# Kernel optimization log

Measured on AMD Instinct MI355X. Metric: run time of the kernel, lower is better.

Reference implementation:

```python
import jax, jax.numpy as jnp
import numpy as np

EPS = 1e-8
LN_EPS = 1e-5
DIM, NHEADS = 512, 8
HEAD_DIM = DIM // NHEADS
SCALE = HEAD_DIM ** -0.5
ROLE_VOCAB = 8


def _layernorm(x, g, b):
    mu = x.mean(-1, keepdims=True)
    var = ((x - mu) ** 2).mean(-1, keepdims=True)
    return (x - mu) * jax.lax.rsqrt(var + LN_EPS) * g + b


def setup_inputs() -> dict:
    key = jax.random.key(0)
    ks = jax.random.split(key, 16)
    B, K, L, D = 8, 4, 1024, DIM
    s = 1.0 / np.sqrt(D)
    return {
        "state_repr": jax.random.normal(ks[0], (B, K, L, D), jnp.float32),
        "residue_mask": jax.random.randint(ks[1], (B, K, L), 0, 2) > 0,
        "state_weights": jax.random.uniform(ks[2], (B, K), jnp.float32),
        "state_roles": jax.random.randint(ks[3], (B, K), 0, ROLE_VOCAB),
        "state_present_mask": jnp.ones((B, K), dtype=bool),
        "role_emb": jax.random.normal(ks[4], (ROLE_VOCAB, D), jnp.float32),
        "Wq": jax.random.normal(ks[5], (D, D), jnp.float32) * s,
        "Wk": jax.random.normal(ks[6], (D, D), jnp.float32) * s,
        "Wv": jax.random.normal(ks[7], (D, D), jnp.float32) * s,
        "Wo": jax.random.normal(ks[8], (D, D), jnp.float32) * s,
        "ln1_g": jnp.ones((3 * D,), jnp.float32),
        "ln1_b": jnp.zeros((3 * D,), jnp.float32),
        "Wg1": jax.random.normal(ks[9], (D, 3 * D), jnp.float32) / np.sqrt(3 * D),
        "bg1": jnp.zeros((D,), jnp.float32),
        "Wg2": jax.random.normal(ks[10], (D, D), jnp.float32) * s,
        "bg2": jnp.zeros((D,), jnp.float32),
        "norm_g": jnp.ones((D,), jnp.float32),
        "norm_b": jnp.zeros((D,), jnp.float32),
    }


def _forward(state_repr, residue_mask, state_weights, state_roles, state_present_mask,
             role_emb, Wq, Wk, Wv, Wo, ln1_g, ln1_b, Wg1, bg1, Wg2, bg2, norm_g, norm_b):
    B, K, L, D = state_repr.shape
    H, hd = NHEADS, HEAD_DIM
    roles = jnp.maximum(state_roles, 0)
    role_e = role_emb[roles][:, :, None, :]                       # [B,K,1,D]
    valid = residue_mask & state_present_mask[:, :, None]          # [B,K,L]

    # normalized state weights
    pres = state_present_mask.astype(jnp.float32)
    w = state_weights.astype(jnp.float32) * pres
    denom = w.sum(1, keepdims=True)
    fallback = pres / jnp.maximum(pres.sum(1, keepdims=True), 1.0)
    nsw = jnp.where(denom > EPS, w / jnp.maximum(denom, EPS), fallback)  # [B,K]

    x = (state_repr + role_e) * valid[..., None]
    x = x.transpose(0, 2, 1, 3)                                    # [B,L,K,D]
    valid_rlk = valid.transpose(0, 2, 1)                           # [B,L,K]

    def proj(W):  # torch Linear: y = x @ W.T
        return (x @ W.T).reshape(B, L, K, H, hd).transpose(0, 1, 3, 2, 4)  # [B,L,H,K,hd]

    q, k, v = proj(Wq), proj(Wk), proj(Wv)
    logits = jnp.einsum('blhqd,blhkd->blhqk', q, k) * SCALE
    logits = logits + jnp.log(jnp.maximum(nsw, EPS))[:, None, None, None, :]
    key_mask = valid_rlk[:, :, None, None, :]                      # [B,L,1,1,K]
    logits = jnp.where(key_mask, logits, -jnp.inf)
    attn = jax.nn.softmax(logits, axis=-1)
    attn = jnp.nan_to_num(attn, nan=0.0, posinf=0.0, neginf=0.0)
    attn_out = jnp.einsum('blhqk,blhkd->blhqd', attn, v)
    attn_out = attn_out.transpose(0, 1, 3, 2, 4).reshape(B, L, K, D)
    attn_out = (attn_out @ Wo.T) * valid_rlk[..., None]

    swr = nsw[:, None, :] * valid_rlk.astype(jnp.float32)          # [B,L,K]
    swr = swr / jnp.maximum(swr.sum(-1, keepdims=True), EPS)
    weighted_mean = jnp.sum(x * swr[..., None], axis=2)            # [B,L,D]
    attn_pooled = jnp.sum(attn_out * swr[..., None], axis=2)

    max_in = jnp.where(valid_rlk[..., None], x, -1e9)
    max_feat = max_in.max(axis=2)
    has_any = valid_rlk.any(axis=2, keepdims=True)
    max_feat = jnp.where(has_any, max_feat, 0.0)

    fusion_base = 0.5 * (attn_pooled + weighted_mean)
    gate_in = jnp.concatenate([attn_pooled, weighted_mean, max_feat], axis=-1)
    h = _layernorm(gate_in, ln1_g, ln1_b)
    h = jax.nn.gelu(h @ Wg1.T + bg1, approximate=False)
    gate = jax.nn.sigmoid(h @ Wg2.T + bg2)
    fused = gate * fusion_base + (1.0 - gate) * max_feat
    fused = _layernorm(fused + weighted_mean, norm_g, norm_b)

    attn_mean = attn.mean(axis=(2, 3))                             # [B,L,K]
    return fused, attn_pooled, weighted_mean, max_feat, attn_mean, nsw


def reference(state_repr, residue_mask, state_weights, state_roles, state_present_mask,
              role_emb, Wq, Wk, Wv, Wo, ln1_g, ln1_b, Wg1, bg1, Wg2, bg2, norm_g, norm_b):
    return _forward(state_repr, residue_mask, state_weights, state_roles, state_present_mask,
                    role_emb, Wq, Wk, Wv, Wo, ln1_g, ln1_b, Wg1, bg1, Wg2, bg2, norm_g, norm_b)
```

## Files before the change

### kernel.cpp

```cpp
#include <hip/hip_runtime.h>
#include <math.h>

#define BB 8
#define KK 4
#define LL 1024
#define DD 512
#define HD 64
#define D3 1536
#define MM (BB*LL*KK)
#define BL (BB*LL)
#define SCALE 0.125f
#define EPSF 1e-8f
#define LN_EPSF 1e-5f

typedef _Float16 hfrag __attribute__((ext_vector_type(8)));
typedef float f32x4 __attribute__((ext_vector_type(4)));

__device__ __forceinline__ unsigned short f2h(float f) {
    _Float16 h = (_Float16)f;
    unsigned short u; __builtin_memcpy(&u, &h, 2); return u;
}
__device__ __forceinline__ float h2f(unsigned short u) {
    _Float16 h; __builtin_memcpy(&h, &u, 2); return (float)h;
}

__device__ __forceinline__ void glds16(const unsigned short* g, unsigned short* l) {
    __builtin_amdgcn_global_load_lds(
        (const __attribute__((address_space(1))) void*)g,
        (__attribute__((address_space(3))) void*)l, 16, 0, 0);
}

__device__ __forceinline__ void nsw_compute(const float* sw, const int* pres,
                                            int b, float* nswv) {
    float w[KK], pr[KK]; float denom = 0.f, ps = 0.f;
    #pragma unroll
    for (int k = 0; k < KK; ++k) {
        pr[k] = pres[b*KK + k] ? 1.f : 0.f;
        w[k]  = sw[b*KK + k] * pr[k];
        denom += w[k]; ps += pr[k];
    }
    #pragma unroll
    for (int k = 0; k < KK; ++k)
        nswv[k] = (denom > EPSF) ? w[k] / fmaxf(denom, EPSF)
                                 : pr[k] / fmaxf(ps, 1.f);
}

#define WSZ 262144
#define OG1 1048576
#define OG2 1835008
#define WTOT 2097152
__global__ __launch_bounds__(256) void cvt_weights(
        const float* __restrict__ Wq, const float* __restrict__ Wk,
        const float* __restrict__ Wv, const float* __restrict__ Wo,
        const float* __restrict__ Wg1, const float* __restrict__ Wg2,
        unsigned short* __restrict__ dst) {
    int t = blockIdx.x * 256 + threadIdx.x;
    int e = t * 4;
    const float* src; int off;
    if      (e < WSZ)    { src = Wq;  off = e; }
    else if (e < 2*WSZ)  { src = Wk;  off = e - WSZ; }
    else if (e < 3*WSZ)  { src = Wv;  off = e - 2*WSZ; }
    else if (e < OG1)    { src = Wo;  off = e - 3*WSZ; }
    else if (e < OG2)    { src = Wg1; off = e - OG1; }
    else                 { src = Wg2; off = e - OG2; }
    float4 v = *(const float4*)(src + off);
    ushort4 o;
    o.x = f2h(v.x); o.y = f2h(v.y); o.z = f2h(v.z); o.w = f2h(v.w);
    *(ushort4*)(dst + e) = o;
}

__global__ __launch_bounds__(256) void buildx_kernel(
        const float* __restrict__ SR, const int* __restrict__ residue,
        const int* __restrict__ pres, const int* __restrict__ roles,
        const float* __restrict__ role_emb, const float* __restrict__ sw,
        unsigned short* __restrict__ Xh, float* __restrict__ rowmask,
        float* __restrict__ out_wm, float* __restrict__ out_mx,
        float* __restrict__ f_nsw) {
    int t  = blockIdx.x * 256 + threadIdx.x;
    int bl = t >> 7;
    int d4 = (t & 127) << 2;
    int b  = bl >> 10, l = bl & 1023;
    float nswv[KK];
    nsw_compute(sw, pres, b, nswv);
    float mk[KK], swr[KK];
    float ssum = 0.f, many = 0.f;
    #pragma unroll
    for (int k = 0; k < KK; ++k) {
        int bk = b*KK + k;
        bool valid = (residue[(size_t)bk*LL + l] != 0) && (pres[bk] != 0);
        mk[k]  = valid ? 1.f : 0.f;
        swr[k] = nswv[k] * mk[k];
        ssum += swr[k]; many += mk[k];
    }
    float inv = 1.f / fmaxf(ssum, EPSF);
    bool hasany = many > 0.5f;
    float wmx = 0.f, wmy = 0.f, wmz = 0.f, wmw = 0.f;
    float mxx = -1e9f, mxy = -1e9f, mxz = -1e9f, mxw = -1e9f;
    #pragma unroll
    for (int k = 0; k < KK; ++k) {
        int bk = b*KK + k;
        int role = roles[bk]; if (role < 0) role = 0;
        float4 sr = *(const float4*)(SR + ((size_t)bk*LL + l)*DD + d4);
        float4 re = *(const float4*)(role_emb + (size_t)role*DD + d4);
        float xx = (sr.x + re.x)*mk[k], xy = (sr.y + re.y)*mk[k];
        float xz = (sr.z + re.z)*mk[k], xw = (sr.w + re.w)*mk[k];
        ushort4 xs; xs.x = f2h(xx); xs.y = f2h(xy); xs.z = f2h(xz); xs.w = f2h(xw);
        *(ushort4*)(Xh + (size_t)(bl*KK + k)*DD + d4) = xs;
        float s = swr[k]*inv;
        wmx = fmaf(xx, s, wmx); wmy = fmaf(xy, s, wmy);
        wmz = fmaf(xz, s, wmz); wmw = fmaf(xw, s, wmw);
        if (mk[k] > 0.5f) {
            mxx = fmaxf(mxx, xx); mxy = fmaxf(mxy, xy);
            mxz = fmaxf(mxz, xz); mxw = fmaxf(mxw, xw);
        }
    }
    if (!hasany) { mxx = mxy = mxz = mxw = 0.f; }
    float4 wmv; wmv.x = wmx; wmv.y = wmy; wmv.z = wmz; wmv.w = wmw;
    float4 mxv; mxv.x = mxx; mxv.y = mxy; mxv.z = mxz; mxv.w = mxw;
    *(float4*)(out_wm + (size_t)bl*DD + d4) = wmv;
    *(float4*)(out_mx + (size_t)bl*DD + d4) = mxv;
    if (d4 == 0) {
        #pragma unroll
        for (int k = 0; k < KK; ++k) rowmask[bl*KK + k] = mk[k];
    }
    if (blockIdx.x == 0 && threadIdx.x < BB*KK) {
        int bb = threadIdx.x >> 2, kk2 = threadIdx.x & 3;
        float nv[KK];
        nsw_compute(sw, pres, bb, nv);
        f_nsw[threadIdx.x] = nv[kk2];
    }
}

__global__ __launch_bounds__(512, 4) void gemm_qkv_8p(
        const unsigned short* __restrict__ A, const unsigned short* __restrict__ W,
        unsigned short* __restrict__ Cbase) {
    __shared__ __align__(16) unsigned short smem[36864];
    const int tid  = threadIdx.x;
    const int wave = tid >> 6, lane = tid & 63;
    const int id = blockIdx.x;
    const int wg = (id & 7) * 192 + (id >> 3);
    const int m0 = (wg / 12) * 256;
    const int n0 = (wg % 12) * 128;
    const int wm = wave >> 1, wn = wave & 1;
    const int fr = lane & 15, q = lane >> 4;
    const int srow = tid >> 2, scc = tid & 3;
    const int sswz = (scc ^ ((srow >> 1) & 3)) << 3;
    const unsigned short* Ag0 = A + (size_t)(m0 + srow)*512 + sswz;
    const unsigned short* Ag1 = Ag0 + (size_t)128*512;
    const unsigned short* Wg0 = W + (size_t)(n0 + srow)*512 + sswz;
    const int lA0 = tid << 3;
    const int lA1 = (tid + 512) << 3;
    int aoff[4], boff[4];
    #pragma unroll
    for (int mf = 0; mf < 4; ++mf) {
        int row = (wm << 6) + (mf << 4) + fr;
        aoff[mf] = (row << 5) + ((q ^ ((row >> 1) & 3)) << 3);
    }
    #pragma unroll
    for (int nf = 0; nf < 4; ++nf) {
        int row = (wn << 6) + (nf << 4) + fr;
        boff[nf] = (row << 5) + ((q ^ ((row >> 1) & 3)) << 3);
    }
    f32x4 acc[4][4] = {};

#define VMWAIT(N) asm volatile("s_waitcnt vmcnt(" #N ")" ::: "memory")
#define STAGE(tt) do { unsigned short* _d = smem + ((tt) % 3) * 12288; \
        const int _ko = (tt) << 5; \
        glds16(Ag0 + _ko, _d + lA0); glds16(Ag1 + _ko, _d + lA1); \
        glds16(Wg0 + _ko, _d + 8192 + lA0); } while (0)
#define MFROW(ai, areg) \
        acc[ai][0] = __builtin_amdgcn_mfma_f32_16x16x32_f16(areg, b0, acc[ai][0], 0, 0, 0); \
        acc[ai][1] = __builtin_amdgcn_mfma_f32_16x16x32_f16(areg, b1, acc[ai][1], 0, 0, 0); \
        acc[ai][2] = __builtin_amdgcn_mfma_f32_16x16x32_f16(areg, b2, acc[ai][2], 0, 0, 0); \
        acc[ai][3] = __builtin_amdgcn_mfma_f32_16x16x32_f16(areg, b3, acc[ai][3], 0, 0, 0);
#define TILE(t, STG, VM) do { \
        const unsigned short* _Ab = smem + ((t) % 3) * 12288; \
        const unsigned short* _Bb = _Ab + 8192; \
        VMWAIT(VM); \
        __builtin_amdgcn_s_barrier(); \
        __builtin_amdgcn_sched_barrier(0); \
        hfrag b0 = *(const hfrag*)(_Bb + boff[0]); \
        hfrag b1 = *(const hfrag*)(_Bb + boff[1]); \
        hfrag b2 = *(const hfrag*)(_Bb + boff[2]); \
        hfrag b3 = *(const hfrag*)(_Bb + boff[3]); \
        hfrag a0_ = *(const hfrag*)(_Ab + aoff[0]); \
        hfrag a1_ = *(const hfrag*)(_Ab + aoff[1]); \
        hfrag a2_ = *(const hfrag*)(_Ab + aoff[2]); \
        hfrag a3_ = *(const hfrag*)(_Ab + aoff[3]); \
        if (STG) STAGE((t) + 2); \
        __builtin_amdgcn_s_setprio(1); \
        MFROW(0, a0_) MFROW(1, a1_) MFROW(2, a2_) MFROW(3, a3_) \
        __builtin_amdgcn_s_setprio(0); \
    } while (0)

    STAGE(0); STAGE(1);
    #pragma unroll
    for (int t = 0; t < 14; ++t) TILE(t, 1, 3);
    TILE(14, 0, 3);
    TILE(15, 0, 0);
#undef TILE
#undef MFROW
#undef STAGE
#undef VMWAIT

    const int gc0 = n0 + (wn << 6);
    const int seg = gc0 >> 9;
    unsigned short* Cs = Cbase + (size_t)seg * ((size_t)MM * 512);
    const int cb = gc0 & 511;
    #pragma unroll
    for (int mf = 0; mf < 4; ++mf) {
        const int grow = m0 + (wm << 6) + (mf << 4) + (q << 2);
        #pragma unroll
        for (int nf = 0; nf < 4; ++nf) {
            const int col = cb + (nf << 4) + fr;
            #pragma unroll
            for (int r = 0; r < 4; ++r)
                Cs[(size_t)(grow + r) * 512 + col] = f2h(acc[mf][nf][r]);
        }
    }
}

__global__ __launch_bounds__(512, 4) void wo_gemm(
        const unsigned short* __restrict__ A,
        const unsigned short* __restrict__ W,
        const float* __restrict__ sw, const int* __restrict__ pres,
        const float* __restrict__ rmask, float* __restrict__ out_ap) {
    __shared__ __align__(16) unsigned short smem[36864];
    const int tid  = threadIdx.x;
    const int wave = tid >> 6, lane = tid & 63;
    const int id = blockIdx.x;
    const int wg = (id & 7) * 64 + (id >> 3);
    const int m0 = (wg >> 2) * 256;
    const int n0 = (wg & 3) * 128;
    const int wm = wave >> 1, wn = wave & 1;
    const int fr = lane & 15, q = lane >> 4;
    const int srow = tid >> 2, scc = tid & 3;
    const int sswz = (scc ^ ((srow >> 1) & 3)) << 3;
    const unsigned short* Ag0 = A + (size_t)(m0 + srow)*512 + sswz;
    const unsigned short* Ag1 = Ag0 + (size_t)128*512;
    const unsigned short* Wg0 = W + (size_t)(n0 + srow)*512 + sswz;
    const int lA0 = tid << 3;
    const int lA1 = (tid + 512) << 3;
    int aoff[4], boff[4];
    #pragma unroll
    for (int mf = 0; mf < 4; ++mf) {
        int row = (wm << 6) + (mf << 4) + fr;
        aoff[mf] = (row << 5) + ((q ^ ((row >> 1) & 3)) << 3);
    }
    #pragma unroll
    for (int nf = 0; nf < 4; ++nf) {
        int row = (wn << 6) + (nf << 4) + fr;
        boff[nf] = (row << 5) + ((q ^ ((row >> 1) & 3)) << 3);
    }
    f32x4 acc[4][4] = {};

#define VMWAIT(N) asm volatile("s_waitcnt vmcnt(" #N ")" ::: "memory")
#define STAGE(tt) do { unsigned short* _d = smem + ((tt) % 3) * 12288; \
        const int _ko = (tt) << 5; \
        glds16(Ag0 + _ko, _d + lA0); glds16(Ag1 + _ko, _d + lA1); \
        glds16(Wg0 + _ko, _d + 8192 + lA0); } while (0)
#define MFROW(ai, areg) \
        acc[ai][0] = __builtin_amdgcn_mfma_f32_16x16x32_f16(areg, b0, acc[ai][0], 0, 0, 0); \
        acc[ai][1] = __builtin_amdgcn_mfma_f32_16x16x32_f16(areg, b1, acc[ai][1], 0, 0, 0); \
        acc[ai][2] = __builtin_amdgcn_mfma_f32_16x16x32_f16(areg, b2, acc[ai][2], 0, 0, 0); \
        acc[ai][3] = __builtin_amdgcn_mfma_f32_16x16x32_f16(areg, b3, acc[ai][3], 0, 0, 0);
#define TILE(t, STG, VM) do { \
        const unsigned short* _Ab = smem + ((t) % 3) * 12288; \
        const unsigned short* _Bb = _Ab + 8192; \
        VMWAIT(VM); \
        __builtin_amdgcn_s_barrier(); \
        __builtin_amdgcn_sched_barrier(0); \
        hfrag b0 = *(const hfrag*)(_Bb + boff[0]); \
        hfrag b1 = *(const hfrag*)(_Bb + boff[1]); \
        hfrag b2 = *(const hfrag*)(_Bb + boff[2]); \
        hfrag b3 = *(const hfrag*)(_Bb + boff[3]); \
        hfrag a0_ = *(const hfrag*)(_Ab + aoff[0]); \
        hfrag a1_ = *(const hfrag*)(_Ab + aoff[1]); \
        hfrag a2_ = *(const hfrag*)(_Ab + aoff[2]); \
        hfrag a3_ = *(const hfrag*)(_Ab + aoff[3]); \
        if (STG) STAGE((t) + 2); \
        __builtin_amdgcn_s_setprio(1); \
        MFROW(0, a0_) MFROW(1, a1_) MFROW(2, a2_) MFROW(3, a3_) \
        __builtin_amdgcn_s_setprio(0); \
    } while (0)

    STAGE(0); STAGE(1);
    #pragma unroll
    for (int t = 0; t < 14; ++t) TILE(t, 1, 3);
    TILE(14, 0, 3);
    TILE(15, 0, 0);
#undef TILE
#undef MFROW
#undef STAGE
#undef VMWAIT

    const int b = (m0 >> 2) >> 10;
    float nv[KK];
    nsw_compute(sw, pres, b, nv);
    #pragma unroll
    for (int mf = 0; mf < 4; ++mf) {
        const int grow = m0 + (wm << 6) + (mf << 4) + (q << 2);
        const int bl = grow >> 2;
        float s4[KK]; float ssum = 0.f;
        #pragma unroll
        for (int k = 0; k < KK; ++k) { s4[k] = nv[k] * rmask[bl*4 + k]; ssum += s4[k]; }
        const float inv = 1.f / fmaxf(ssum, EPSF);
        #pragma unroll
        for (int nf = 0; nf < 4; ++nf) {
            const int col = n0 + (wn << 6) + (nf << 4) + fr;
            float ap = 0.f;
            #pragma unroll
            for (int r = 0; r < KK; ++r) ap = fmaf(s4[r]*inv, acc[mf][nf][r], ap);
            out_ap[(size_t)bl*512 + col] = ap;
        }
    }
}

__global__ __launch_bounds__(256) void ln1_kernel(
        const float* __restrict__ ap, const float* __restrict__ wm,
        const float* __restrict__ mx, const float* __restrict__ g,
        const float* __restrict__ bvec, unsigned short* __restrict__ hin) {
    const int bl = blockIdx.x * 4 + (threadIdx.x >> 6);
    const int lane = threadIdx.x & 63;
    const int c0 = lane * 8;
    float4 v[3][2];
    const float* srcs[3] = { ap + (size_t)bl*512 + c0,
                             wm + (size_t)bl*512 + c0,
                             mx + (size_t)bl*512 + c0 };
    float s = 0.f, s2 = 0.f;
    #pragma unroll
    for (int sg = 0; sg < 3; ++sg) {
        v[sg][0] = *(const float4*)(srcs[sg]);
        v[sg][1] = *(const float4*)(srcs[sg] + 4);
        #pragma unroll
        for (int e = 0; e < 8; ++e) {
            float x = ((const float*)v[sg])[e];
            s += x; s2 += x*x;
        }
    }
    #pragma unroll
    for (int o = 1; o < 64; o <<= 1) {
        s  += __shfl_xor(s,  o, 64);
        s2 += __shfl_xor(s2, o, 64);
    }
    const float mu = s * (1.f/(float)D3);
    const float var = s2 * (1.f/(float)D3) - mu*mu;
    const float rstd = rsqrtf(var + LN_EPSF);
    #pragma unroll
    for (int sg = 0; sg < 3; ++sg) {
        const int gofs = sg*512 + c0;
        #pragma unroll
        for (int h = 0; h < 2; ++h) {
            float4 g4 = *(const float4*)(g + gofs + h*4);
            float4 b4 = *(const float4*)(bvec + gofs + h*4);
            const float* sv = (const float*)&v[sg][h];
            ushort4 o4;
            o4.x = f2h((sv[0]-mu)*rstd*g4.x + b4.x);
            o4.y = f2h((sv[1]-mu)*rstd*g4.y + b4.y);
            o4.z = f2h((sv[2]-mu)*rstd*g4.z + b4.z);
            o4.w = f2h((sv[3]-mu)*rstd*g4.w + b4.w);
            *(ushort4*)(hin + (size_t)bl*D3 + gofs + h*4) = o4;
        }
    }
}

__global__ __launch_bounds__(256, 3) void gemm_g1(
        const unsigned short* __restrict__ A, const unsigned short* __restrict__ W,
        unsigned short* __restrict__ C, const float* __restrict__ bias) {
    __shared__ __align__(16) unsigned short smem[24576];
    const int tid  = threadIdx.x;
    const int wave = tid >> 6, lane = tid & 63;
    const int id = blockIdx.x;
    const int wg = (id & 7) * 32 + (id >> 3);
    const int m0 = (wg >> 2) * 128;
    const int n0 = (wg & 3) * 128;
    const int wm = wave >> 1, wn = wave & 1;
    const int fr = lane & 15, q = lane >> 4;
    const int srow = tid >> 2, scc = tid & 3;
    const int sswz = (scc ^ ((srow >> 1) & 3)) << 3;
    const unsigned short* Ag0 = A + (size_t)(m0 + srow)*D3 + sswz;
    const unsigned short* Ag1 = Ag0 + (size_t)64*D3;
    const unsigned short* Wg0 = W + (size_t)(n0 + srow)*D3 + sswz;
    const unsigned short* Wg1p = Wg0 + (size_t)64*D3;
    const int lA0 = tid << 3;
    const int lA1 = (tid + 256) << 3;
    int aoff[4], boff[4];
    #pragma unroll
    for (int mf = 0; mf < 4; ++mf) {
        int row = (wm << 6) + (mf << 4) + fr;
        aoff[mf] = (row << 5) + ((q ^ ((row >> 1) & 3)) << 3);
    }
    #pragma unroll
    for (int nf = 0; nf < 4; ++nf) {
        int row = (wn << 6) + (nf << 4) + fr;
        boff[nf] = (row << 5) + ((q ^ ((row >> 1) & 3)) << 3);
    }
    f32x4 acc[4][4] = {};

#define VMWAIT(N) asm volatile("s_waitcnt vmcnt(" #N ")" ::: "memory")
#define STAGE(tt) do { unsigned short* _d = smem + ((tt) % 3) * 8192; \
        const int _ko = (tt) << 5; \
        glds16(Ag0 + _ko, _d + lA0); glds16(Ag1 + _ko, _d + lA1); \
        glds16(Wg0 + _ko, _d + 4096 + lA0); glds16(Wg1p + _ko, _d + 4096 + lA1); } while (0)
#define MFROW(ai, areg) \
        acc[ai][0] = __builtin_amdgcn_mfma_f32_16x16x32_f16(areg, b0, acc[ai][0], 0, 0, 0); \
        acc[ai][1] = __builtin_amdgcn_mfma_f32_16x16x32_f16(areg, b1, acc[ai][1], 0, 0, 0); \
        acc[ai][2] = __builtin_amdgcn_mfma_f32_16x16x32_f16(areg, b2, acc[ai][2], 0, 0, 0); \
        acc[ai][3] = __builtin_amdgcn_mfma_f32_16x16x32_f16(areg, b3, acc[ai][3], 0, 0, 0);
#define TILE(t, STG, VM) do { \
        const unsigned short* _Ab = smem + ((t) % 3) * 8192; \
        const unsigned short* _Bb = _Ab + 4096; \
        VMWAIT(VM); \
        __builtin_amdgcn_s_barrier(); \
        __builtin_amdgcn_sched_barrier(0); \
        hfrag b0 = *(const hfrag*)(_Bb + boff[0]); \
        hfrag b1 = *(const hfrag*)(_Bb + boff[1]); \
        hfrag b2 = *(const hfrag*)(_Bb + boff[2]); \
        hfrag b3 = *(const hfrag*)(_Bb + boff[3]); \
        hfrag a0_ = *(const hfrag*)(_Ab + aoff[0]); \
        hfrag a1_ = *(const hfrag*)(_Ab + aoff[1]); \
        hfrag a2_ = *(const hfrag*)(_Ab + aoff[2]); \
        hfrag a3_ = *(const hfrag*)(_Ab + aoff[3]); \
        if (STG) STAGE((t) + 2); \
        __builtin_amdgcn_s_setprio(1); \
        MFROW(0, a0_) MFROW(1, a1_) MFROW(2, a2_) MFROW(3, a3_) \
        __builtin_amdgcn_s_setprio(0); \
    } while (0)

    STAGE(0); STAGE(1);
    #pragma unroll 3
    for (int t = 0; t < 46; ++t) TILE(t, 1, 4);
    TILE(46, 0, 4);
    TILE(47, 0, 0);
#undef TILE
#undef MFROW
#undef STAGE
#undef VMWAIT

    #pragma unroll
    for (int mf = 0; mf < 4; ++mf) {
        const int grow = m0 + (wm << 6) + (mf << 4) + (q << 2);
        #pragma unroll
        for (int nf = 0; nf < 4; ++nf) {
            const int col = n0 + (wn << 6) + (nf << 4) + fr;
            const float bv = bias[col];
            #pragma unroll
            for (int r = 0; r < 4; ++r) {
                float v = acc[mf][nf][r] + bv;
                v = 0.5f * v * (1.f + erff(v * 0.70710678118654752f));
                C[(size_t)(grow + r) * 512 + col] = f2h(v);
            }
        }
    }
}

__global__ __launch_bounds__(256, 3) void wg2_gemm(
        const unsigned short* __restrict__ A,
        const unsigned short* __restrict__ W,
        const float* __restrict__ bg2,
        const float* __restrict__ in_ap, const float* __restrict__ in_wm,
        const float* __restrict__ in_mx, float* __restrict__ pre) {
    __shared__ __align__(16) unsigned short smem[24576];
    const int tid  = threadIdx.x;
    const int wave = tid >> 6, lane = tid & 63;
    const int id = blockIdx.x;
    const int wg = (id & 7) * 32 + (id >> 3);
    const int m0 = (wg >> 2) * 128;
    const int n0 = (wg & 3) * 128;
    const int wm = wave >> 1, wn = wave & 1;
    const int fr = lane & 15, q = lane >> 4;
    const int srow = tid >> 2, scc = tid & 3;
    const int sswz = (scc ^ ((srow >> 1) & 3)) << 3;
    const unsigned short* Ag0 = A + (size_t)(m0 + srow)*512 + sswz;
    const unsigned short* Ag1 = Ag0 + (size_t)64*512;
    const unsigned short* Wg0 = W + (size_t)(n0 + srow)*512 + sswz;
    const unsigned short* Wg1p = Wg0 + (size_t)64*512;
    const int lA0 = tid << 3;
    const int lA1 = (tid + 256) << 3;
    int aoff[4], boff[4];
    #pragma unroll
    for (int mf = 0; mf < 4; ++mf) {
        int row = (wm << 6) + (mf << 4) + fr;
        aoff[mf] = (row << 5) + ((q ^ ((row >> 1) & 3)) << 3);
    }
    #pragma unroll
    for (int nf = 0; nf < 4; ++nf) {
        int row = (wn << 6) + (nf << 4) + fr;
        boff[nf] = (row << 5) + ((q ^ ((row >> 1) & 3)) << 3);
    }
    f32x4 acc[4][4] = {};

#define VMWAIT(N) asm volatile("s_waitcnt vmcnt(" #N ")" ::: "memory")
#define STAGE(tt) do { unsigned short* _d = smem + ((tt) % 3) * 8192; \
        const int _ko = (tt) << 5; \
        glds16(Ag0 + _ko, _d + lA0); glds16(Ag1 + _ko, _d + lA1); \
        glds16(Wg0 + _ko, _d + 4096 + lA0); glds16(Wg1p + _ko, _d + 4096 + lA1); } while (0)
#define MFROW(ai, areg) \
        acc[ai][0] = __builtin_amdgcn_mfma_f32_16x16x32_f16(areg, b0, acc[ai][0], 0, 0, 0); \
        acc[ai][1] = __builtin_amdgcn_mfma_f32_16x16x32_f16(areg, b1, acc[ai][1], 0, 0, 0); \
        acc[ai][2] = __builtin_amdgcn_mfma_f32_16x16x32_f16(areg, b2, acc[ai][2], 0, 0, 0); \
        acc[ai][3] = __builtin_amdgcn_mfma_f32_16x16x32_f16(areg, b3, acc[ai][3], 0, 0, 0);
#define TILE(t, STG, VM) do { \
        const unsigned short* _Ab = smem + ((t) % 3) * 8192; \
        const unsigned short* _Bb = _Ab + 4096; \
        VMWAIT(VM); \
        __builtin_amdgcn_s_barrier(); \
        __builtin_amdgcn_sched_barrier(0); \
        hfrag b0 = *(const hfrag*)(_Bb + boff[0]); \
        hfrag b1 = *(const hfrag*)(_Bb + boff[1]); \
        hfrag b2 = *(const hfrag*)(_Bb + boff[2]); \
        hfrag b3 = *(const hfrag*)(_Bb + boff[3]); \
        hfrag a0_ = *(const hfrag*)(_Ab + aoff[0]); \
        hfrag a1_ = *(const hfrag*)(_Ab + aoff[1]); \
        hfrag a2_ = *(const hfrag*)(_Ab + aoff[2]); \
        hfrag a3_ = *(const hfrag*)(_Ab + aoff[3]); \
        if (STG) STAGE((t) + 2); \
        __builtin_amdgcn_s_setprio(1); \
        MFROW(0, a0_) MFROW(1, a1_) MFROW(2, a2_) MFROW(3, a3_) \
        __builtin_amdgcn_s_setprio(0); \
    } while (0)

    STAGE(0); STAGE(1);
    #pragma unroll
    for (int t = 0; t < 14; ++t) TILE(t, 1, 4);
    TILE(14, 0, 4);
    TILE(15, 0, 0);
#undef TILE
#undef MFROW
#undef STAGE
#undef VMWAIT

    #pragma unroll
    for (int mf = 0; mf < 4; ++mf) {
        const int grow = m0 + (wm << 6) + (mf << 4) + (q << 2);
        #pragma unroll
        for (int nf = 0; nf < 4; ++nf) {
            const int col = n0 + (wn << 6) + (nf << 4) + fr;
            const float bv = bg2[col];
            #pragma unroll
            for (int r = 0; r < 4; ++r) {
                const int row = grow + r;
                float g = 1.f / (1.f + expf(-(acc[mf][nf][r] + bv)));
                float ap = in_ap[(size_t)row*512 + col];
                float wmv = in_wm[(size_t)row*512 + col];
                float mxv = in_mx[(size_t)row*512 + col];
                pre[(size_t)row*512 + col] = g*0.5f*(ap + wmv) + (1.f - g)*mxv + wmv;
            }
        }
    }
}

__global__ __launch_bounds__(256) void final_ln_kernel(
        const float* __restrict__ pre, const float* __restrict__ ng,
        const float* __restrict__ nb, float* __restrict__ fused) {
    const int row = blockIdx.x * 4 + (threadIdx.x >> 6);
    const int lane = threadIdx.x & 63;
    const int c0 = lane * 8;
    float4 p0 = *(const float4*)(pre + (size_t)row*512 + c0);
    float4 p1 = *(const float4*)(pre + (size_t)row*512 + c0 + 4);
    float s = 0.f, s2 = 0.f;
    const float* pv = (const float*)&p0;
    #pragma unroll
    for (int e = 0; e < 4; ++e) { s += pv[e]; s2 += pv[e]*pv[e]; }
    pv = (const float*)&p1;
    #pragma unroll
    for (int e = 0; e < 4; ++e) { s += pv[e]; s2 += pv[e]*pv[e]; }
    #pragma unroll
    for (int o = 1; o < 64; o <<= 1) {
        s  += __shfl_xor(s,  o, 64);
        s2 += __shfl_xor(s2, o, 64);
    }
    const float mu = s * (1.f/(float)DD);
    const float var = s2 * (1.f/(float)DD) - mu*mu;
    const float rstd = rsqrtf(var + LN_EPSF);
    float4 g0 = *(const float4*)(ng + c0), g1 = *(const float4*)(ng + c0 + 4);
    float4 b0 = *(const float4*)(nb + c0), b1 = *(const float4*)(nb + c0 + 4);
    float4 o0, o1;
    o0.x = (p0.x-mu)*rstd*g0.x + b0.x; o0.y = (p0.y-mu)*rstd*g0.y + b0.y;
    o0.z = (p0.z-mu)*rstd*g0.z + b0.z; o0.w = (p0.w-mu)*rstd*g0.w + b0.w;
    o1.x = (p1.x-mu)*rstd*g1.x + b1.x; o1.y = (p1.y-mu)*rstd*g1.y + b1.y;
    o1.z = (p1.z-mu)*rstd*g1.z + b1.z; o1.w = (p1.w-mu)*rstd*g1.w + b1.w;
    *(float4*)(fused + (size_t)row*512 + c0) = o0;
    *(float4*)(fused + (size_t)row*512 + c0 + 4) = o1;
}

__global__ __launch_bounds__(256) void attn_kernel(
        unsigned short* Qb ,
        const unsigned short* __restrict__ Kb, const unsigned short* __restrict__ Vb,
        const float* __restrict__ sw, const int* __restrict__ pres,
        const float* __restrict__ rowmask,
        float* __restrict__ attn_mean_out) {
    __shared__ float att[128];
    __shared__ float lw[KK], mk[KK];
    int bl = blockIdx.x, b = bl >> 10, mb = bl * KK;
    int tid = threadIdx.x;
    if (tid < KK) {
        float nv[KK];
        nsw_compute(sw, pres, b, nv);
        lw[tid] = logf(fmaxf(nv[tid], EPSF));
        mk[tid] = rowmask[mb + tid];
    }
    __syncthreads();
    if (tid < 128) {
        int h = tid >> 4, i = (tid >> 2) & 3, j = tid & 3;
        const unsigned short* qp = Qb + (size_t)(mb + i)*DD + h*HD;
        const unsigned short* kp = Kb + (size_t)(mb + j)*DD + h*HD;
        float s = 0.f;
        #pragma unroll
        for (int c = 0; c < 8; ++c) {
            hfrag qv = *(const hfrag*)(qp + c*8);
            hfrag kv = *(const hfrag*)(kp + c*8);
            #pragma unroll
            for (int e = 0; e < 8; ++e)
                s = fmaf((float)qv[e], (float)kv[e], s);
        }
        float lg = s * SCALE + lw[j];
        att[tid] = (mk[j] > 0.5f) ? lg : -INFINITY;
    }
    __syncthreads();
    if (tid < 32) {
        int base = tid * 4;
        float l0 = att[base], l1 = att[base+1], l2 = att[base+2], l3 = att[base+3];
        float m = fmaxf(fmaxf(l0, l1), fmaxf(l2, l3));
        if (m == -INFINITY) {
            att[base] = att[base+1] = att[base+2] = att[base+3] = 0.f;
        } else {
            float e0 = expf(l0 - m), e1 = expf(l1 - m), e2 = expf(l2 - m), e3 = expf(l3 - m);
            float inv = 1.f / (e0 + e1 + e2 + e3);
            att[base] = e0*inv; att[base+1] = e1*inv; att[base+2] = e2*inv; att[base+3] = e3*inv;
        }
    }
    __syncthreads();
    if (tid < KK) {
        float s = 0.f;
        for (int hi = 0; hi < 32; ++hi) s += att[hi*4 + tid];
        attn_mean_out[(size_t)bl*KK + tid] = s * (1.f/32.f);
    }
    #pragma unroll
    for (int p = 0; p < 4; ++p) {
        int idx = p*256 + tid;
        int i = idx >> 8, d2 = (idx & 255) << 1, h = d2 >> 6;
        float s0 = 0.f, s1 = 0.f;
        #pragma unroll
        for (int j = 0; j < KK; ++j) {
            float aj = att[h*16 + i*4 + j];
            ushort2 vv = *(const ushort2*)(Vb + (size_t)(mb + j)*DD + d2);
            s0 = fmaf(aj, h2f(vv.x), s0);
            s1 = fmaf(aj, h2f(vv.y), s1);
        }
        ushort2 o; o.x = f2h(s0); o.y = f2h(s1);
        *(ushort2*)(Qb + (size_t)(mb + i)*DD + d2) = o;
    }
}

extern "C" void kernel_launch(void* const* d_in, const int* in_sizes, int n_in,
                              void* d_out, int out_size, void* d_ws, size_t ws_size,
                              hipStream_t stream) {
    const float* SR      = (const float*)d_in[0];
    const int*   residue = (const int*)d_in[1];
    const float* sw      = (const float*)d_in[2];
    const int*   roles   = (const int*)d_in[3];
    const int*   pres    = (const int*)d_in[4];
    const float* role_emb= (const float*)d_in[5];
    const float* Wq      = (const float*)d_in[6];
    const float* Wk      = (const float*)d_in[7];
    const float* Wv      = (const float*)d_in[8];
    const float* Wo      = (const float*)d_in[9];
    const float* ln1_g   = (const float*)d_in[10];
    const float* ln1_b   = (const float*)d_in[11];
    const float* Wg1     = (const float*)d_in[12];
    const float* bg1     = (const float*)d_in[13];
    const float* Wg2     = (const float*)d_in[14];
    const float* bg2     = (const float*)d_in[15];
    const float* norm_g  = (const float*)d_in[16];
    const float* norm_b  = (const float*)d_in[17];

    float* out = (float*)d_out;
    const size_t BLD = (size_t)BL * DD;
    float* f_fused = out;
    float* f_ap    = out + BLD;
    float* f_wm    = out + 2*BLD;
    float* f_mx    = out + 3*BLD;
    float* f_am    = out + 4*BLD;
    float* f_nsw   = out + 4*BLD + (size_t)BL*KK;

    char* base = (char*)d_ws;
    const size_t MD2 = (size_t)MM * DD * 2;
    unsigned short* Xh = (unsigned short*)(base);
    unsigned short* Qh = (unsigned short*)(base + MD2);
    unsigned short* Kh = (unsigned short*)(base + 2*MD2);
    unsigned short* Vh = (unsigned short*)(base + 3*MD2);
    unsigned short* Wb = (unsigned short*)(base + 4*MD2);
    float* rmask = (float*)(base + 4*MD2 + (size_t)WTOT*2);
    unsigned short* AOh  = Qh;
    unsigned short* Hin  = Vh;
    unsigned short* Hbuf = Xh;
    float* preb = (float*)Kh;
    const unsigned short* Wqkv = Wb;
    const unsigned short* Woh  = Wb + 3*WSZ;
    const unsigned short* Wg1h = Wb + OG1;
    const unsigned short* Wg2h = Wb + OG2;

    dim3 blk(256);

    cvt_weights<<<WTOT/1024, blk, 0, stream>>>(Wq, Wk, Wv, Wo, Wg1, Wg2, Wb);
    buildx_kernel<<<(BL*128)/256, blk, 0, stream>>>(SR, residue, pres, roles, role_emb,
                                                    sw, Xh, rmask, f_wm, f_mx, f_nsw);

    gemm_qkv_8p<<<dim3(1536), dim3(512), 0, stream>>>(Xh, Wqkv, Qh);

    attn_kernel<<<BL, blk, 0, stream>>>(Qh, Kh, Vh, sw, pres, rmask, f_am);

    wo_gemm<<<dim3(512), dim3(512), 0, stream>>>(
        AOh, Woh, sw, pres, rmask, f_ap);

    ln1_kernel<<<dim3(BL/4), blk, 0, stream>>>(
        f_ap, f_wm, f_mx, ln1_g, ln1_b, Hin);

    gemm_g1<<<dim3(256), blk, 0, stream>>>(Hin, Wg1h, Hbuf, bg1);

    wg2_gemm<<<dim3(256), blk, 0, stream>>>(
        Hbuf, Wg2h, bg2, f_ap, f_wm, f_mx, preb);

    final_ln_kernel<<<dim3(BL/4), blk, 0, stream>>>(
        preb, norm_g, norm_b, f_fused);
}
```

Baseline: 335.2 us.

## Pre-swizzle X and QKV weights into MFMA fragment layout, load directly without LDS

The build-X kernel and the weight conversion now write X and Wq/Wk/Wv in a 16-row fragment-major layout matching the MFMA operand order. The QKV GEMM is replaced by an LDS-free kernel with 256 threads and a 128x128 tile, where each wave loads its own A and B fragments straight from global memory with a two-deep register double buffer. This removes LDS staging, barriers and swizzle math, but loses cross-wave sharing of tiles, so global and L2 traffic per FLOP doubles.

```diff
diff --git a/kernel.cpp b/kernel.cpp
--- a/kernel.cpp
+++ b/kernel.cpp
@@ -56,13 +56,26 @@
         unsigned short* __restrict__ dst) {
     int t = blockIdx.x * 256 + threadIdx.x;
     int e = t * 4;
+    if (e < 3*WSZ) {
+        const float* src; int off;
+        if      (e < WSZ)   { src = Wq; off = e; }
+        else if (e < 2*WSZ) { src = Wk; off = e - WSZ; }
+        else                { src = Wv; off = e - 2*WSZ; }
+        float4 v = *(const float4*)(src + off);
+        ushort4 o;
+        o.x = f2h(v.x); o.y = f2h(v.y); o.z = f2h(v.z); o.w = f2h(v.w);
+        const int n = e >> 9;
+        const int k = e & 511;
+        const int nb = n >> 4, fr = n & 15;
+        const int kt = k >> 5, q = (k >> 3) & 3, e0 = k & 7;
+        const size_t di = ((size_t)(nb*16 + kt)*64 + q*16 + fr)*8 + e0;
+        *(ushort4*)(dst + di) = o;
+        return;
+    }
     const float* src; int off;
-    if      (e < WSZ)    { src = Wq;  off = e; }
-    else if (e < 2*WSZ)  { src = Wk;  off = e - WSZ; }
-    else if (e < 3*WSZ)  { src = Wv;  off = e - 2*WSZ; }
-    else if (e < OG1)    { src = Wo;  off = e - 3*WSZ; }
-    else if (e < OG2)    { src = Wg1; off = e - OG1; }
-    else                 { src = Wg2; off = e - OG2; }
+    if      (e < OG1) { src = Wo;  off = e - 3*WSZ; }
+    else if (e < OG2) { src = Wg1; off = e - OG1; }
+    else              { src = Wg2; off = e - OG2; }
     float4 v = *(const float4*)(src + off);
     ushort4 o;
     o.x = f2h(v.x); o.y = f2h(v.y); o.z = f2h(v.z); o.w = f2h(v.w);
@@ -94,6 +107,7 @@
     }
     float inv = 1.f / fmaxf(ssum, EPSF);
     bool hasany = many > 0.5f;
+    const int kt = d4 >> 5, fq = (d4 >> 3) & 3, e0 = d4 & 7;
     float wmx = 0.f, wmy = 0.f, wmz = 0.f, wmw = 0.f;
     float mxx = -1e9f, mxy = -1e9f, mxz = -1e9f, mxw = -1e9f;
     #pragma unroll
@@ -105,7 +119,10 @@
         float xx = (sr.x + re.x)*mk[k], xy = (sr.y + re.y)*mk[k];
         float xz = (sr.z + re.z)*mk[k], xw = (sr.w + re.w)*mk[k];
         ushort4 xs; xs.x = f2h(xx); xs.y = f2h(xy); xs.z = f2h(xz); xs.w = f2h(xw);
-        *(ushort4*)(Xh + (size_t)(bl*KK + k)*DD + d4) = xs;
+        const int m = bl*KK + k;
+        const int mb = m >> 4, fr = m & 15;
+        const size_t di = ((size_t)(mb*16 + kt)*64 + fq*16 + fr)*8 + e0;
+        *(ushort4*)(Xh + di) = xs;
         float s = swr[k]*inv;
         wmx = fmaf(xx, s, wmx); wmy = fmaf(xy, s, wmy);
         wmz = fmaf(xz, s, wmz); wmw = fmaf(xw, s, wmw);
@@ -131,16 +148,81 @@
     }
 }
 
-__global__ __launch_bounds__(512, 4) void gemm_qkv_8p(
-        const unsigned short* __restrict__ A, const unsigned short* __restrict__ W,
+__global__ __launch_bounds__(256, 3) void gemm_qkv_frag(
+        const unsigned short* __restrict__ Af, const unsigned short* __restrict__ Wf,
         unsigned short* __restrict__ Cbase) {
+    const int tid  = threadIdx.x;
+    const int wave = tid >> 6, lane = tid & 63;
+    const int id = blockIdx.x;
+    const int wg = (id & 7) * 384 + (id >> 3);
+    const int m0 = (wg / 12) * 128;
+    const int n0 = (wg % 12) * 128;
+    const int wm = wave >> 1, wn = wave & 1;
+    const int fr = lane & 15, q = lane >> 4;
+    const unsigned short* ap[4];
+    const unsigned short* bp[4];
+    #pragma unroll
+    for (int i = 0; i < 4; ++i) {
+        const int mb = (m0 >> 4) + wm*4 + i;
+        const int nb = (n0 >> 4) + wn*4 + i;
+        ap[i] = Af + (size_t)mb*16*512 + lane*8;
+        bp[i] = Wf + (size_t)nb*16*512 + lane*8;
+    }
+    hfrag a[2][4], b[2][4];
+    f32x4 acc[4][4] = {};
+
+#define LDGEN(g, t) do { \
+        _Pragma("unroll") \
+        for (int i = 0; i < 4; ++i) { \
+            a[g][i] = *(const hfrag*)(ap[i] + (t)*512); \
+            b[g][i] = *(const hfrag*)(bp[i] + (t)*512); \
+        } } while (0)
+
+    LDGEN(0, 0);
+    LDGEN(1, 1);
+    #pragma unroll
+    for (int t = 0; t < 16; ++t) {
+        const int g = t & 1;
+        __builtin_amdgcn_s_setprio(1);
+        #pragma unroll
+        for (int i = 0; i < 4; ++i)
+            #pragma unroll
+            for (int j = 0; j < 4; ++j)
+                acc[i][j] = __builtin_amdgcn_mfma_f32_16x16x32_f16(a[g][i], b[g][j], acc[i][j], 0, 0, 0);
+        __builtin_amdgcn_s_setprio(0);
+        if (t < 14) LDGEN(g, t + 2);
+    }
+#undef LDGEN
+
+    const int gc0 = n0 + (wn << 6);
+    const int seg = gc0 >> 9;
+    unsigned short* Cs = Cbase + (size_t)seg * ((size_t)MM * 512);
+    const int cb = gc0 & 511;
+    #pragma unroll
+    for (int mf = 0; mf < 4; ++mf) {
+        const int grow = m0 + (wm << 6) + (mf << 4) + (q << 2);
+        #pragma unroll
+        for (int nf = 0; nf < 4; ++nf) {
+            const int col = cb + (nf << 4) + fr;
+            #pragma unroll
+            for (int r = 0; r < 4; ++r)
+                Cs[(size_t)(grow + r) * 512 + col] = f2h(acc[mf][nf][r]);
+        }
+    }
+}
+
+__global__ __launch_bounds__(512, 4) void wo_gemm(
+        const unsigned short* __restrict__ A,
+        const unsigned short* __restrict__ W,
+        const float* __restrict__ sw, const int* __restrict__ pres,
+        const float* __restrict__ rmask, float* __restrict__ out_ap) {
     __shared__ __align__(16) unsigned short smem[36864];
     const int tid  = threadIdx.x;
     const int wave = tid >> 6, lane = tid & 63;
     const int id = blockIdx.x;
-    const int wg = (id & 7) * 192 + (id >> 3);
-    const int m0 = (wg / 12) * 256;
-    const int n0 = (wg % 12) * 128;
+    const int wg = (id & 7) * 64 + (id >> 3);
+    const int m0 = (wg >> 2) * 256;
+    const int n0 = (wg & 3) * 128;
     const int wm = wave >> 1, wn = wave & 1;
     const int fr = lane & 15, q = lane >> 4;
     const int srow = tid >> 2, scc = tid & 3;
@@ -203,97 +285,6 @@
 #undef STAGE
 #undef VMWAIT
 
-    const int gc0 = n0 + (wn << 6);
-    const int seg = gc0 >> 9;
-    unsigned short* Cs = Cbase + (size_t)seg * ((size_t)MM * 512);
-    const int cb = gc0 & 511;
-    #pragma unroll
-    for (int mf = 0; mf < 4; ++mf) {
-        const int grow = m0 + (wm << 6) + (mf << 4) + (q << 2);
-        #pragma unroll
-        for (int nf = 0; nf < 4; ++nf) {
-            const int col = cb + (nf << 4) + fr;
-            #pragma unroll
-            for (int r = 0; r < 4; ++r)
-                Cs[(size_t)(grow + r) * 512 + col] = f2h(acc[mf][nf][r]);
-        }
-    }
-}
-
-__global__ __launch_bounds__(512, 4) void wo_gemm(
-        const unsigned short* __restrict__ A,
-        const unsigned short* __restrict__ W,
-        const float* __restrict__ sw, const int* __restrict__ pres,
-        const float* __restrict__ rmask, float* __restrict__ out_ap) {
-    __shared__ __align__(16) unsigned short smem[36864];
-    const int tid  = threadIdx.x;
-    const int wave = tid >> 6, lane = tid & 63;
-    const int id = blockIdx.x;
-    const int wg = (id & 7) * 64 + (id >> 3);
-    const int m0 = (wg >> 2) * 256;
-    const int n0 = (wg & 3) * 128;
-    const int wm = wave >> 1, wn = wave & 1;
-    const int fr = lane & 15, q = lane >> 4;
-    const int srow = tid >> 2, scc = tid & 3;
-    const int sswz = (scc ^ ((srow >> 1) & 3)) << 3;
-    const unsigned short* Ag0 = A + (size_t)(m0 + srow)*512 + sswz;
-    const unsigned short* Ag1 = Ag0 + (size_t)128*512;
-    const unsigned short* Wg0 = W + (size_t)(n0 + srow)*512 + sswz;
-    const int lA0 = tid << 3;
-    const int lA1 = (tid + 512) << 3;
-    int aoff[4], boff[4];
-    #pragma unroll
-    for (int mf = 0; mf < 4; ++mf) {
-        int row = (wm << 6) + (mf << 4) + fr;
-        aoff[mf] = (row << 5) + ((q ^ ((row >> 1) & 3)) << 3);
-    }
-    #pragma unroll
-    for (int nf = 0; nf < 4; ++nf) {
-        int row = (wn << 6) + (nf << 4) + fr;
-        boff[nf] = (row << 5) + ((q ^ ((row >> 1) & 3)) << 3);
-    }
-    f32x4 acc[4][4] = {};
-
-#define VMWAIT(N) asm volatile("s_waitcnt vmcnt(" #N ")" ::: "memory")
-#define STAGE(tt) do { unsigned short* _d = smem + ((tt) % 3) * 12288; \
-        const int _ko = (tt) << 5; \
-        glds16(Ag0 + _ko, _d + lA0); glds16(Ag1 + _ko, _d + lA1); \
-        glds16(Wg0 + _ko, _d + 8192 + lA0); } while (0)
-#define MFROW(ai, areg) \
-        acc[ai][0] = __builtin_amdgcn_mfma_f32_16x16x32_f16(areg, b0, acc[ai][0], 0, 0, 0); \
-        acc[ai][1] = __builtin_amdgcn_mfma_f32_16x16x32_f16(areg, b1, acc[ai][1], 0, 0, 0); \
-        acc[ai][2] = __builtin_amdgcn_mfma_f32_16x16x32_f16(areg, b2, acc[ai][2], 0, 0, 0); \
-        acc[ai][3] = __builtin_amdgcn_mfma_f32_16x16x32_f16(areg, b3, acc[ai][3], 0, 0, 0);
-#define TILE(t, STG, VM) do { \
-        const unsigned short* _Ab = smem + ((t) % 3) * 12288; \
-        const unsigned short* _Bb = _Ab + 8192; \
-        VMWAIT(VM); \
-        __builtin_amdgcn_s_barrier(); \
-        __builtin_amdgcn_sched_barrier(0); \
-        hfrag b0 = *(const hfrag*)(_Bb + boff[0]); \
-        hfrag b1 = *(const hfrag*)(_Bb + boff[1]); \
-        hfrag b2 = *(const hfrag*)(_Bb + boff[2]); \
-        hfrag b3 = *(const hfrag*)(_Bb + boff[3]); \
-        hfrag a0_ = *(const hfrag*)(_Ab + aoff[0]); \
-        hfrag a1_ = *(const hfrag*)(_Ab + aoff[1]); \
-        hfrag a2_ = *(const hfrag*)(_Ab + aoff[2]); \
-        hfrag a3_ = *(const hfrag*)(_Ab + aoff[3]); \
-        if (STG) STAGE((t) + 2); \
-        __builtin_amdgcn_s_setprio(1); \
-        MFROW(0, a0_) MFROW(1, a1_) MFROW(2, a2_) MFROW(3, a3_) \
-        __builtin_amdgcn_s_setprio(0); \
-    } while (0)
-
-    STAGE(0); STAGE(1);
-    #pragma unroll
-    for (int t = 0; t < 14; ++t) TILE(t, 1, 3);
-    TILE(14, 0, 3);
-    TILE(15, 0, 0);
-#undef TILE
-#undef MFROW
-#undef STAGE
-#undef VMWAIT
-
     const int b = (m0 >> 2) >> 10;
     float nv[KK];
     nsw_compute(sw, pres, b, nv);
@@ -707,7 +698,7 @@
     buildx_kernel<<<(BL*128)/256, blk, 0, stream>>>(SR, residue, pres, roles, role_emb,
                                                     sw, Xh, rmask, f_wm, f_mx, f_nsw);
 
-    gemm_qkv_8p<<<dim3(1536), dim3(512), 0, stream>>>(Xh, Wqkv, Qh);
+    gemm_qkv_frag<<<dim3(3072), blk, 0, stream>>>(Xh, Wqkv, Qh);
 
     attn_kernel<<<BL, blk, 0, stream>>>(Qh, Kh, Vh, sw, pres, rmask, f_am);
 
```

Measured after the change: 382.9 us. 14.2% more time.
